# Optimization experiments

Hardware: AMD Instinct MI355X
Metric: run time of the kernel (lower is better)

Reference implementation:

```python
import jax, jax.numpy as jnp
import numpy as np

FEATURE_MAPS = [38, 19, 10, 5, 3, 1]
NUM_ANCHORS = [4, 6, 6, 6, 4, 4]
SCALES = (0.2, 0.9)
RATIOS = np.array([1.0, 1.0, 2.0, 3.0, 0.5, 1.0 / 3.0])
BACKGROUND_ID = 0
EPS = 1e-6


def _generate_anchors():
    """Replicates AnchorManager._generate_anchors: order is (i, j, k)."""
    all_anchors = []
    for size, n in zip(FEATURE_MAPS, NUM_ANCHORS):
        scales = np.linspace(SCALES[0], SCALES[1], n)
        ratios = RATIOS[:n]
        rs = np.sqrt(ratios)
        w = scales * rs          # [n]
        h = scales / rs          # [n]
        cy = (np.arange(size) + 0.5) / size  # i -> rows (varies slowest)
        cx = (np.arange(size) + 0.5) / size  # j -> cols
        grid = np.zeros((size, size, n, 4), dtype=np.float64)
        grid[..., 0] = cx[None, :, None]
        grid[..., 1] = cy[:, None, None]
        grid[..., 2] = w[None, None, :]
        grid[..., 3] = h[None, None, :]
        all_anchors.append(grid.reshape(-1, 4))
    return np.concatenate(all_anchors).astype(np.float32)  # [A, 4] cxcywh


def _cxcywh_to_xyxy(b):
    cxy, wh = b[..., :2], b[..., 2:]
    return jnp.concatenate([cxy - wh / 2, cxy + wh / 2], axis=-1)


def _xyxy_to_cxcywh(b):
    xy1, xy2 = b[..., :2], b[..., 2:]
    return jnp.concatenate([(xy1 + xy2) / 2, xy2 - xy1], axis=-1)


def setup_inputs() -> dict:
    key = jax.random.key(0)
    k1, k2, k3 = jax.random.split(key, 3)
    B, N = 64, 100
    # valid normalized xyxy gt boxes
    xy = jax.random.uniform(k1, (B, N, 2), dtype=jnp.float32) * 0.8
    wh = jax.random.uniform(k2, (B, N, 2), dtype=jnp.float32) * 0.19 + 0.01
    gt_boxes = jnp.concatenate([xy, xy + wh], axis=-1)
    gt_labels = jax.random.randint(k3, (B, N), 1, 81, dtype=jnp.int64 if jax.config.jax_enable_x64 else jnp.int32).astype(jnp.int32)
    anchors_cxcywh = jnp.asarray(_generate_anchors())          # [A, 4]
    anchors_xyxy = _cxcywh_to_xyxy(anchors_cxcywh)             # [A, 4]
    return {
        "gt_labels": gt_labels,
        "gt_boxes": gt_boxes,
        "anchors_cxcywh": anchors_cxcywh,
        "anchors_xyxy": anchors_xyxy,
    }


def _iou(anchors_xyxy, gt_boxes):
    # anchors_xyxy: [A,4], gt_boxes: [B,N,4] -> iou [B,A,N]
    a = anchors_xyxy[None, :, None, :]   # [1,A,1,4]
    g = gt_boxes[:, None, :, :]          # [B,1,N,4]
    lt = jnp.maximum(a[..., :2], g[..., :2])
    rb = jnp.minimum(a[..., 2:], g[..., 2:])
    wh = jnp.clip(rb - lt, 0.0)
    inter = wh[..., 0] * wh[..., 1]
    area_a = (a[..., 2] - a[..., 0]) * (a[..., 3] - a[..., 1])
    area_g = (g[..., 2] - g[..., 0]) * (g[..., 3] - g[..., 1])
    return (inter / (area_a + area_g - inter)).astype(jnp.float32)


def reference(gt_labels, gt_boxes, anchors_cxcywh, anchors_xyxy):
    B, N = gt_boxes.shape[0], gt_boxes.shape[1]
    A = anchors_cxcywh.shape[0]

    gt_boxes_coco = _xyxy_to_cxcywh(gt_boxes)                  # [B,N,4]
    ious = _iou(anchors_xyxy, gt_boxes)                        # [B,A,N]

    anchors_gt = jnp.max(ious, axis=-1)                        # [B,A]
    anchors_gt_idx = jnp.argmax(ious, axis=-1)                 # [B,A]
    gt_anchors_idx = jnp.argmax(ious, axis=-2)                 # [B,N] best anchor per gt

    # force-match: each gt claims its best anchor
    b_idx = jnp.arange(B)[:, None]
    range_n = jnp.broadcast_to(jnp.arange(N), (B, N))
    anchors_gt_idx = anchors_gt_idx.at[b_idx, gt_anchors_idx].set(range_n)
    anchors_gt = anchors_gt.at[b_idx, gt_anchors_idx].set(2.0)

    pos_mask = anchors_gt > 0.5                                # [B,A]

    matched_gtb = jnp.take_along_axis(gt_boxes_coco, anchors_gt_idx[..., None], axis=1)  # [B,A,4]
    matched_labels = jnp.take_along_axis(gt_labels, anchors_gt_idx, axis=1)              # [B,A]
    encoded_labels = jnp.where(pos_mask, matched_labels, BACKGROUND_ID)

    anc = anchors_cxcywh[None]                                 # [1,A,4]
    enc_cxy = (matched_gtb[..., :2] - anc[..., :2]) / anc[..., 2:]
    enc_wh = jnp.log((matched_gtb[..., 2:] + EPS) / (anc[..., 2:] + EPS))
    encoded = jnp.concatenate([enc_cxy, enc_wh], axis=-1)      # [B,A,4]

    return encoded_labels, encoded, pos_mask
```

## Files before the change

kernel.cpp:

```cpp
#include <hip/hip_runtime.h>
#include <math.h>

#pragma clang fp contract(off)


#define AA 8732
#define NN 100
#define BB 64
#define NPB 4
#define EPS_F 1e-6f

__global__ __launch_bounds__(256) void col_argmax_kernel(
        const float4* __restrict__ gt_boxes,
        const float4* __restrict__ anchors_xyxy,
        int* __restrict__ gt_anchors_idx)
{
    const int b  = blockIdx.y;
    const int n0 = blockIdx.x * NPB;
    const int tid = threadIdx.x;

    float4 g[NPB];
    float  area_g[NPB];
    #pragma unroll
    for (int j = 0; j < NPB; j++) {
        g[j] = gt_boxes[b * NN + n0 + j];
        area_g[j] = (g[j].z - g[j].x) * (g[j].w - g[j].y);
    }

    float bv[NPB];
    int   bi[NPB];
    #pragma unroll
    for (int j = 0; j < NPB; j++) { bv[j] = -1.0f; bi[j] = 0x7fffffff; }

    #pragma unroll 2
    for (int a = tid; a < AA; a += 256) {
        float4 an = anchors_xyxy[a];
        float area_a = (an.z - an.x) * (an.w - an.y);
        #pragma unroll
        for (int j = 0; j < NPB; j++) {
            float ltx = fmaxf(an.x, g[j].x);
            float lty = fmaxf(an.y, g[j].y);
            float rbx = fminf(an.z, g[j].z);
            float rby = fminf(an.w, g[j].w);
            float w = fmaxf(rbx - ltx, 0.0f);
            float h = fmaxf(rby - lty, 0.0f);
            float inter = w * h;
            float iou = inter / (area_a + area_g[j] - inter);
            if (iou > bv[j] || (iou == bv[j] && a < bi[j])) { bv[j] = iou; bi[j] = a; }
        }
    }

    __shared__ float sval[NPB][256];
    __shared__ int   sidx[NPB][256];
    #pragma unroll
    for (int j = 0; j < NPB; j++) { sval[j][tid] = bv[j]; sidx[j][tid] = bi[j]; }
    __syncthreads();
    for (int s = 128; s > 0; s >>= 1) {
        if (tid < s) {
            #pragma unroll
            for (int j = 0; j < NPB; j++) {
                float v2 = sval[j][tid + s];
                int   i2 = sidx[j][tid + s];
                if (v2 > sval[j][tid] || (v2 == sval[j][tid] && i2 < sidx[j][tid])) {
                    sval[j][tid] = v2;
                    sidx[j][tid] = i2;
                }
            }
        }
        __syncthreads();
    }
    if (tid < NPB) gt_anchors_idx[b * NN + n0 + tid] = sidx[tid][0];
}

__global__ __launch_bounds__(256) void encode_kernel(
        const int* __restrict__ gt_labels,
        const float4* __restrict__ gt_boxes,
        const float4* __restrict__ anchors_cxcywh,
        const float4* __restrict__ anchors_xyxy,
        const int* __restrict__ gt_anchors_idx,
        float* __restrict__ out)
{
    const int b = blockIdx.y;
    const int tid = threadIdx.x;
    const int a = blockIdx.x * 256 + tid;

    __shared__ float4 sg[NN];
    __shared__ float  sarea[NN];
    __shared__ int    sgi[NN];
    __shared__ int    slab[NN];
    if (tid < NN) {
        float4 gg = gt_boxes[b * NN + tid];
        sg[tid]    = gg;
        sarea[tid] = (gg.z - gg.x) * (gg.w - gg.y);
        sgi[tid]   = gt_anchors_idx[b * NN + tid];
        slab[tid]  = gt_labels[b * NN + tid];
    }
    __syncthreads();

    if (a >= AA) return;

    const float4 axy = anchors_xyxy[a];
    const float area_a = (axy.z - axy.x) * (axy.w - axy.y);

    float bv = -1.0f;
    int bi = 0;
    int ovr = -1;
    #pragma unroll 4
    for (int n = 0; n < NN; n++) {
        float4 gg = sg[n];
        float area_g = sarea[n];
        float ltx = fmaxf(axy.x, gg.x);
        float lty = fmaxf(axy.y, gg.y);
        float rbx = fminf(axy.z, gg.z);
        float rby = fminf(axy.w, gg.w);
        float w = fmaxf(rbx - ltx, 0.0f);
        float h = fmaxf(rby - lty, 0.0f);
        float inter = w * h;
        float iou = inter / (area_a + area_g - inter);
        if (iou > bv) { bv = iou; bi = n; }
        if (sgi[n] == a) ovr = n;
    }

    float val;
    int idx;
    if (ovr >= 0) { idx = ovr; val = 2.0f; }
    else          { idx = bi;  val = bv; }
    const bool pos = val > 0.5f;

    const float4 gg = sg[idx];
    const float gcx = (gg.x + gg.z) * 0.5f;
    const float gcy = (gg.y + gg.w) * 0.5f;
    const float gw  = gg.z - gg.x;
    const float gh  = gg.w - gg.y;

    const float4 anc = anchors_cxcywh[a];
    const float ecx = (gcx - anc.x) / anc.z;
    const float ecy = (gcy - anc.y) / anc.w;
    const float ew  = logf((gw + EPS_F) / (anc.z + EPS_F));
    const float eh  = logf((gh + EPS_F) / (anc.w + EPS_F));

    const size_t BA = (size_t)BB * AA;
    const size_t base = (size_t)b * AA + a;

    out[base] = pos ? (float)slab[idx] : 0.0f;
    ((float4*)(out + BA))[base] = make_float4(ecx, ecy, ew, eh);
    out[5 * BA + base] = pos ? 1.0f : 0.0f;
}

extern "C" void kernel_launch(void* const* d_in, const int* in_sizes, int n_in,
                              void* d_out, int out_size, void* d_ws, size_t ws_size,
                              hipStream_t stream) {
    const int*    gt_labels    = (const int*)d_in[0];
    const float4* gt_boxes     = (const float4*)d_in[1];
    const float4* anchors_cxcy = (const float4*)d_in[2];
    const float4* anchors_xyxy = (const float4*)d_in[3];
    float* out = (float*)d_out;

    int* gt_anchors_idx = (int*)d_ws;

    dim3 grid1(NN / NPB, BB);
    col_argmax_kernel<<<grid1, 256, 0, stream>>>(gt_boxes, anchors_xyxy,
                                                 gt_anchors_idx);

    dim3 grid2((AA + 255) / 256, BB);
    encode_kernel<<<grid2, 256, 0, stream>>>(gt_labels, gt_boxes, anchors_cxcy,
                                             anchors_xyxy, gt_anchors_idx, out);
}
```

Baseline: 154.0 us.

## Compute IoU once, fuse row and column argmax via wave-reduced packed atomics

The IoU matrix was computed twice before: once in a column-argmax kernel over anchors and again in the encode kernel. Now one pass computes IoU per anchor against all gts. It keeps the row argmax in registers and updates the per-gt column max with packed 64-bit (iou, inverse index) atomicMax. A shared-memory threshold skips wave reductions that cannot win, and each wave starts at a staggered gt to reduce atomic contention. A scatter kernel then marks force-matched anchors, and encode reads the stored results through scratch space in the output buffer, at the cost of an extra memset, an extra launch and many global atomics.

Result: slower. 178.1 us (+15.7%).

```diff
diff --git a/kernel.cpp b/kernel.cpp
--- a/kernel.cpp
+++ b/kernel.cpp
@@ -7,77 +7,103 @@
 #define AA 8732
 #define NN 100
 #define BB 64
-#define NPB 4
 #define EPS_F 1e-6f
+#define OVR_FLAG 0x10000
 
-__global__ __launch_bounds__(256) void col_argmax_kernel(
+__global__ __launch_bounds__(256) void iou_pass_kernel(
         const float4* __restrict__ gt_boxes,
         const float4* __restrict__ anchors_xyxy,
-        int* __restrict__ gt_anchors_idx)
+        unsigned long long* __restrict__ colmax,
+        float* __restrict__ out_val,
+        int* __restrict__ out_slot)
 {
-    const int b  = blockIdx.y;
-    const int n0 = blockIdx.x * NPB;
+    const int b = blockIdx.y;
     const int tid = threadIdx.x;
+    const int a = blockIdx.x * 256 + tid;
+    const bool valid = (a < AA);
+    const int ac = valid ? a : (AA - 1);
 
-    float4 g[NPB];
-    float  area_g[NPB];
-    #pragma unroll
-    for (int j = 0; j < NPB; j++) {
-        g[j] = gt_boxes[b * NN + n0 + j];
-        area_g[j] = (g[j].z - g[j].x) * (g[j].w - g[j].y);
+    __shared__ float4   sg[NN];
+    __shared__ float    sarea[NN];
+    __shared__ unsigned scurhi[NN];
+
+    if (tid < NN) {
+        float4 g = gt_boxes[b * NN + tid];
+        sg[tid] = g;
+        sarea[tid] = (g.z - g.x) * (g.w - g.y);
+        scurhi[tid] = 1u;
     }
+    __syncthreads();
 
-    float bv[NPB];
-    int   bi[NPB];
-    #pragma unroll
-    for (int j = 0; j < NPB; j++) { bv[j] = -1.0f; bi[j] = 0x7fffffff; }
+    const float4 axy = anchors_xyxy[ac];
+    const float area_a = (axy.z - axy.x) * (axy.w - axy.y);
+    const unsigned lowkey = (unsigned)(AA - ac);
 
-    #pragma unroll 2
-    for (int a = tid; a < AA; a += 256) {
-        float4 an = anchors_xyxy[a];
-        float area_a = (an.z - an.x) * (an.w - an.y);
-        #pragma unroll
-        for (int j = 0; j < NPB; j++) {
-            float ltx = fmaxf(an.x, g[j].x);
-            float lty = fmaxf(an.y, g[j].y);
-            float rbx = fminf(an.z, g[j].z);
-            float rby = fminf(an.w, g[j].w);
-            float w = fmaxf(rbx - ltx, 0.0f);
-            float h = fmaxf(rby - lty, 0.0f);
-            float inter = w * h;
-            float iou = inter / (area_a + area_g[j] - inter);
-            if (iou > bv[j] || (iou == bv[j] && a < bi[j])) { bv[j] = iou; bi[j] = a; }
+    float bv = -1.0f;
+    int bi = NN;
+
+    int nstart = ((tid >> 6) * 25 + (blockIdx.x * 7) % 25) % NN;
+
+    for (int t = 0; t < NN; t++) {
+        int n = nstart + t;
+        if (n >= NN) n -= NN;
+
+        float4 g = sg[n];
+        float area_g = sarea[n];
+        float ltx = fmaxf(axy.x, g.x);
+        float lty = fmaxf(axy.y, g.y);
+        float rbx = fminf(axy.z, g.z);
+        float rby = fminf(axy.w, g.w);
+        float w = fmaxf(rbx - ltx, 0.0f);
+        float h = fmaxf(rby - lty, 0.0f);
+        float inter = w * h;
+        float iou = inter / (area_a + area_g - inter);
+
+        if (iou > bv || (iou == bv && n < bi)) { bv = iou; bi = n; }
+
+        unsigned qb = __float_as_uint(iou);
+        bool pass = valid && (qb >= scurhi[n]);
+        if (__any((int)pass)) {
+            unsigned long long v = valid
+                ? ((((unsigned long long)qb) << 32) | (unsigned long long)lowkey)
+                : 0ull;
+            #pragma unroll
+            for (int off = 32; off > 0; off >>= 1) {
+                unsigned long long o = __shfl_xor(v, off);
+                v = (o > v) ? o : v;
+            }
+            if ((tid & 63) == 0) {
+                atomicMax(colmax + b * NN + n, v);
+                atomicMax(&scurhi[n], (unsigned)(v >> 32));
+            }
         }
     }
 
-    __shared__ float sval[NPB][256];
-    __shared__ int   sidx[NPB][256];
-    #pragma unroll
-    for (int j = 0; j < NPB; j++) { sval[j][tid] = bv[j]; sidx[j][tid] = bi[j]; }
-    __syncthreads();
-    for (int s = 128; s > 0; s >>= 1) {
-        if (tid < s) {
-            #pragma unroll
-            for (int j = 0; j < NPB; j++) {
-                float v2 = sval[j][tid + s];
-                int   i2 = sidx[j][tid + s];
-                if (v2 > sval[j][tid] || (v2 == sval[j][tid] && i2 < sidx[j][tid])) {
-                    sval[j][tid] = v2;
-                    sidx[j][tid] = i2;
-                }
-            }
+    if (valid) {
+        const size_t base = (size_t)b * AA + a;
+        out_val[base] = bv;
+        out_slot[base] = bi;
+    }
+}
+
+__global__ void scatter_kernel(const unsigned long long* __restrict__ colmax,
+                               int* __restrict__ out_slot) {
+    const int b = blockIdx.x;
+    const int n = threadIdx.x;
+    if (n < NN) {
+        unsigned long long v = colmax[b * NN + n];
+        unsigned low = (unsigned)(v & 0xFFFFFFFFull);
+        if (low >= 1u && low <= (unsigned)AA) {
+            int idx = AA - (int)low;
+            atomicMax(&out_slot[(size_t)b * AA + idx], OVR_FLAG + n);
         }
-        __syncthreads();
     }
-    if (tid < NPB) gt_anchors_idx[b * NN + n0 + tid] = sidx[tid][0];
 }
 
 __global__ __launch_bounds__(256) void encode_kernel(
         const int* __restrict__ gt_labels,
         const float4* __restrict__ gt_boxes,
         const float4* __restrict__ anchors_cxcywh,
-        const float4* __restrict__ anchors_xyxy,
-        const int* __restrict__ gt_anchors_idx,
         float* __restrict__ out)
 {
     const int b = blockIdx.y;
@@ -85,62 +111,36 @@
     const int a = blockIdx.x * 256 + tid;
 
     __shared__ float4 sg[NN];
-    __shared__ float  sarea[NN];
-    __shared__ int    sgi[NN];
     __shared__ int    slab[NN];
     if (tid < NN) {
-        float4 gg = gt_boxes[b * NN + tid];
-        sg[tid]    = gg;
-        sarea[tid] = (gg.z - gg.x) * (gg.w - gg.y);
-        sgi[tid]   = gt_anchors_idx[b * NN + tid];
-        slab[tid]  = gt_labels[b * NN + tid];
+        sg[tid]   = gt_boxes[b * NN + tid];
+        slab[tid] = gt_labels[b * NN + tid];
     }
     __syncthreads();
-
     if (a >= AA) return;
 
-    const float4 axy = anchors_xyxy[a];
-    const float area_a = (axy.z - axy.x) * (axy.w - axy.y);
+    const size_t BA = (size_t)BB * AA;
+    const size_t base = (size_t)b * AA + a;
 
-    float bv = -1.0f;
-    int bi = 0;
-    int ovr = -1;
-    #pragma unroll 4
-    for (int n = 0; n < NN; n++) {
-        float4 gg = sg[n];
-        float area_g = sarea[n];
-        float ltx = fmaxf(axy.x, gg.x);
-        float lty = fmaxf(axy.y, gg.y);
-        float rbx = fminf(axy.z, gg.z);
-        float rby = fminf(axy.w, gg.w);
-        float w = fmaxf(rbx - ltx, 0.0f);
-        float h = fmaxf(rby - lty, 0.0f);
-        float inter = w * h;
-        float iou = inter / (area_a + area_g - inter);
-        if (iou > bv) { bv = iou; bi = n; }
-        if (sgi[n] == a) ovr = n;
-    }
+    float bv = out[base];
+    int s = ((const int*)(out + 5 * BA))[base];
 
-    float val;
-    int idx;
-    if (ovr >= 0) { idx = ovr; val = 2.0f; }
-    else          { idx = bi;  val = bv; }
+    int idx; float val;
+    if (s >= OVR_FLAG) { idx = s - OVR_FLAG; val = 2.0f; }
+    else               { idx = s;            val = bv;   }
     const bool pos = val > 0.5f;
 
-    const float4 gg = sg[idx];
-    const float gcx = (gg.x + gg.z) * 0.5f;
-    const float gcy = (gg.y + gg.w) * 0.5f;
-    const float gw  = gg.z - gg.x;
-    const float gh  = gg.w - gg.y;
+    const float4 g = sg[idx];
+    const float gcx = (g.x + g.z) * 0.5f;
+    const float gcy = (g.y + g.w) * 0.5f;
+    const float gw  = g.z - g.x;
+    const float gh  = g.w - g.y;
 
     const float4 anc = anchors_cxcywh[a];
     const float ecx = (gcx - anc.x) / anc.z;
     const float ecy = (gcy - anc.y) / anc.w;
     const float ew  = logf((gw + EPS_F) / (anc.z + EPS_F));
     const float eh  = logf((gh + EPS_F) / (anc.w + EPS_F));
-
-    const size_t BA = (size_t)BB * AA;
-    const size_t base = (size_t)b * AA + a;
 
     out[base] = pos ? (float)slab[idx] : 0.0f;
     ((float4*)(out + BA))[base] = make_float4(ecx, ecy, ew, eh);
@@ -156,13 +156,15 @@
     const float4* anchors_xyxy = (const float4*)d_in[3];
     float* out = (float*)d_out;
 
-    int* gt_anchors_idx = (int*)d_ws;
+    const size_t BA = (size_t)BB * AA;
+    unsigned long long* colmax = (unsigned long long*)(out + BA);
+    int* slot = (int*)(out + 5 * BA);
 
-    dim3 grid1(NN / NPB, BB);
-    col_argmax_kernel<<<grid1, 256, 0, stream>>>(gt_boxes, anchors_xyxy,
-                                                 gt_anchors_idx);
+    hipMemsetAsync(colmax, 0, (size_t)BB * NN * sizeof(unsigned long long), stream);
 
-    dim3 grid2((AA + 255) / 256, BB);
-    encode_kernel<<<grid2, 256, 0, stream>>>(gt_labels, gt_boxes, anchors_cxcy,
-                                             anchors_xyxy, gt_anchors_idx, out);
+    dim3 grid((AA + 255) / 256, BB);
+    iou_pass_kernel<<<grid, 256, 0, stream>>>(gt_boxes, anchors_xyxy, colmax,
+                                              out, slot);
+    scatter_kernel<<<BB, 128, 0, stream>>>(colmax, slot);
+    encode_kernel<<<grid, 256, 0, stream>>>(gt_labels, gt_boxes, anchors_cxcy, out);
 }
```
